# Kernel optimization log

Measured on AMD Instinct MI355X. Metric: run time of the kernel, lower is better.

Reference implementation:

```python
import jax, jax.numpy as jnp
import numpy as np

# Model dims (must match init_kwargs / input_specs)
D = 64          # hidden_dims
L = 2           # num_layer
R = 50          # num_relation
N_RAW = 20000   # num_nodes (module uses num_nodes+1 internally, node 0 = padding)
N = N_RAW + 1
A = 6           # max_arity
E = 30000       # num hyperedges
B = 4           # batch size
C = 500         # candidates per query (1 true + negatives, all differ in one slot)
ARITY = 4       # query arity (constant per batch, as the asserts require)
FEAT = 2 * D    # feature_dim = hidden_dims + input_dim
LN_EPS = 1e-5


def _sinusoidal_pos(max_arity, dim):
    # static_positional_encoding: frozen sinusoidal table, row 0 zeroed (padding)
    pos = np.arange(max_arity + 1, dtype=np.float64)[:, None]
    i = np.arange(dim, dtype=np.float64)[None, :]
    angle = pos / np.power(10000.0, (2.0 * np.floor(i / 2.0)) / dim)
    pe = np.where(np.arange(dim)[None, :] % 2 == 0, np.sin(angle), np.cos(angle))
    pe[0] = 0.0
    return jnp.asarray(pe, jnp.float32)


def setup_inputs() -> dict:
    key = jax.random.key(0)
    ks = jax.random.split(key, 16)
    # --- query batch: one corrupted slot per row, constant relation / arity per row ---
    base = jax.random.randint(ks[0], (B, A), 1, N)                       # entity ids 1..N-1
    base = base * (jnp.arange(A)[None, :] < ARITY)                       # pad slots >= arity -> node 0
    pos_corrupt = jax.random.randint(ks[1], (B,), 0, ARITY)              # which slot differs
    cand = (jnp.arange(C)[None, :] + jax.random.randint(ks[2], (B, 1), 1, N)) % (N - 1) + 1  # [B,C] distinct ids
    ent = jnp.broadcast_to(base[:, None, :], (B, C, A))
    entities_idx = jnp.where(jnp.arange(A)[None, None, :] == pos_corrupt[:, None, None],
                             cand[:, :, None], ent).astype(jnp.int64)    # [B,C,A]
    r_idx = jnp.broadcast_to(jax.random.randint(ks[3], (B, 1), 0, R), (B, C)).astype(jnp.int64)
    arity = jnp.full((B, C), ARITY, dtype=jnp.int64)
    # --- hypergraph: padded incidence lists ---
    edge_ar = jax.random.randint(ks[4], (E,), 2, A + 1)
    edge_list = (jax.random.randint(ks[5], (E, A), 1, N)
                 * (jnp.arange(A)[None, :] < edge_ar[:, None])).astype(jnp.int64)  # [E,A], 0-padded
    rel_list = jax.random.randint(ks[6], (E,), 0, R).astype(jnp.int64)
    # --- parameters ---
    sD = 1.0 / np.sqrt(D)
    sF = 1.0 / np.sqrt(FEAT)
    params = dict(
        query_emb=jax.random.normal(ks[7], (R, D), jnp.float32) * sD,
        rel_emb=jax.random.normal(ks[8], (L, R, D), jnp.float32) * sD,   # per-layer relation table (dependent=False)
        W_agg=jax.random.normal(ks[9], (L, D, D), jnp.float32) * sD,
        W_self=jax.random.normal(ks[10], (L, D, D), jnp.float32) * sD,
        b_lin=jnp.zeros((L, D), jnp.float32),
        ln_g=jnp.ones((L, D), jnp.float32),
        ln_b=jnp.zeros((L, D), jnp.float32),
        W1=jax.random.normal(ks[11], (FEAT, FEAT), jnp.float32) * sF,
        b1=jnp.zeros((FEAT,), jnp.float32),
        W2=jax.random.normal(ks[12], (FEAT, 1), jnp.float32) * sF,
        b2=jnp.zeros((1,), jnp.float32),
    )
    return dict(r_idx=r_idx, entities_idx=entities_idx, arity=arity,
                edge_list=edge_list, rel_list=rel_list,
                pos_table=_sinusoidal_pos(A, D), **params)


def _layer_norm(x, g, b):
    mu = x.mean(-1, keepdims=True)
    var = jnp.mean(jnp.square(x - mu), -1, keepdims=True)
    return (x - mu) * jax.lax.rsqrt(var + LN_EPS) * g + b


def reference(r_idx, entities_idx, arity, edge_list, rel_list, pos_table,
              query_emb, rel_emb, W_agg, W_self, b_lin, ln_g, ln_b, W1, b1, W2, b2):
    all_idx = jnp.transpose(entities_idx, (0, 2, 1))                 # [B,A,C]
    mask_for_diff = jnp.all(all_idx[:, :, :1] == all_idx, axis=-1)   # [B,A] True = slot constant
    pos_search = jnp.argmax(~mask_for_diff, axis=1)                  # [B] corrupted slot
    query = query_emb[r_idx[:, 0]]                                   # [B,D]

    rng = jnp.arange(A)
    valid = rng[None, :] < arity[:, :1]                              # [B,A]
    result = (valid & (rng[None, :] != pos_search[:, None])).astype(all_idx.dtype)  # [B,A]
    idx_ws = all_idx[:, :, 0] * result                               # [B,A] node ids (0 = skip)
    b_ix = jnp.arange(r_idx.shape[0])

    # init: scatter-add relation query + positional encodings onto the query entities
    init = jnp.zeros((r_idx.shape[0], N, D), jnp.float32)
    init = init.at[b_ix[:, None], idx_ws].add(
        jnp.broadcast_to(query[:, None, :], (r_idx.shape[0], A, D)))
    pos_src = pos_table[result * (rng + 1)[None, :]]                 # [B,A,D]
    init = init.at[b_ix[:, None], idx_ws].add(pos_src)
    init = init.at[:, 0, :].set(0.0)                                 # padding node stays 0

    ev = (edge_list != 0)                                            # [E,A] valid slots
    pos_e = pos_table[jnp.arange(1, A + 1)[None, :] * ev]            # [E,A,D] (pos_table[0]=0)
    evf = ev[None, :, :, None].astype(jnp.float32)

    layer_input = init
    for l in range(L):
        h_e = layer_input[:, edge_list]                              # [B,E,A,D] gather
        r_e = rel_emb[l][rel_list]                                   # [E,D]
        m = (h_e + pos_e[None]) * r_e[None, :, None, :] * evf        # per-slot message factor
        msg = (m.sum(axis=2, keepdims=True) - m) * evf               # sum over other slots j != i
        agg = jnp.zeros_like(layer_input).at[:, edge_list].add(msg)  # scatter-add to nodes
        agg = agg.at[:, 0, :].set(0.0)
        out = agg @ W_agg[l] + layer_input @ W_self[l] + b_lin[l]
        out = _layer_norm(out, ln_g[l], ln_b[l])                     # (dropout = identity at eval)
        hidden = jax.nn.relu(out)
        layer_input = hidden + layer_input                           # short_cut residual

    # gather candidate rows (exactly one differing slot per batch row -> jit-friendly)
    cand = jnp.take_along_axis(all_idx, pos_search[:, None, None], axis=1)[:, 0, :]  # [B,C]
    feat_nodes = layer_input[b_ix[:, None], cand]                    # [B,C,D]
    feat = jnp.concatenate(
        [feat_nodes, jnp.broadcast_to(query[:, None, :], feat_nodes.shape)], axis=-1)  # [B,C,2D]
    score = (jax.nn.relu(feat @ W1 + b1) @ W2 + b2)[..., 0]          # [B,C]
    return score
```

## Files before the change

### kernel.cpp

```cpp
#include <hip/hip_runtime.h>

#define D_ 64
#define L_ 2
#define R_ 50
#define N_ 20001
#define A_ 6
#define E_ 30000
#define B_ 4
#define C_ 500
#define FEAT_ 128
#define SC_CAP 8192
#define DCAP 64

__device__ __forceinline__ float rlane(float v, int k) {
  return __builtin_bit_cast(float, __builtin_amdgcn_readlane(__builtin_bit_cast(int, v), k));
}
__device__ __forceinline__ float wave_sum(float v) {
#pragma unroll
  for (int off = 32; off; off >>= 1) v += __shfl_xor(v, off);
  return v;
}
__device__ __forceinline__ float sel6(float p0, float p1, float p2, float p3,
                                      float p4, float p5, int a) {
  float r = p0;
  r = (a == 1) ? p1 : r; r = (a == 2) ? p2 : r; r = (a == 3) ? p3 : r;
  r = (a == 4) ? p4 : r; r = (a == 5) ? p5 : r;
  return r;
}


#define ZQUADS 15007

__global__ void zero_kernel(float4* __restrict__ z) {
  int i = blockIdx.x * blockDim.x + threadIdx.x;
  if (i < ZQUADS) z[i] = make_float4(0.f, 0.f, 0.f, 0.f);
}


#define IB_INIT 4
#define IB_EMASK ((E_ + 255) / 256)
#define IB_BUCKET ((E_ * A_ + 255) / 256)
#define IB_BLOCKS (IB_INIT + IB_EMASK + IB_BUCKET)

__global__ __launch_bounds__(256) void init_bucket_kernel(
    const int* __restrict__ r_idx, const int* __restrict__ ents,
    const int* __restrict__ arity, const float* __restrict__ pos_table,
    const float* __restrict__ query_emb, const int* __restrict__ edge_list,
    int* __restrict__ seednode, float* __restrict__ seedvec,
    int* __restrict__ dirtyA, int* __restrict__ dirty_n, int* __restrict__ meta,
    int* __restrict__ deg, int* __restrict__ bucket, int* __restrict__ emask) {
  __shared__ int diff[A_];
  int bid = blockIdx.x, t = threadIdx.x;
  if (bid < IB_INIT) {
    int b = bid;
    if (t < A_) diff[t] = 0;
    __syncthreads();
#pragma unroll
    for (int a = 0; a < A_; ++a) {
      int v0 = ents[(b * C_) * A_ + a];
      int dd = 0;
      for (int c = t; c < C_; c += 256) dd |= (ents[(b * C_ + c) * A_ + a] != v0);
      if (dd) diff[a] = 1;
    }
    __syncthreads();
    int ps = 0;
    for (int a = A_ - 1; a >= 0; --a) if (diff[a]) ps = a;
    int qr = r_idx[b * C_];
    if (t == 0) { meta[b] = ps; meta[B_ + b] = qr; }
    int ar = arity[b * C_];
    int lane = t & 63;
    for (int a = (t >> 6); a < A_; a += 4) {
      int slot = b * A_ + a;
      if (a < ar && a != ps) {
        int n = ents[(b * C_) * A_ + a];
        seedvec[slot * D_ + lane] = query_emb[qr * D_ + lane] + pos_table[(a + 1) * D_ + lane];
        if (lane == 0) {
          seednode[slot] = n;
          atomicOr(&dirtyA[n], 1 << b);
          atomicOr(&dirty_n[n], 1 << b);
        }
      } else {
        if (lane == 0) seednode[slot] = 0;
      }
    }
  } else if (bid < IB_INIT + IB_EMASK) {
    int e = (bid - IB_INIT) * 256 + t;
    if (e < E_) {
      int msk = 0;
#pragma unroll
      for (int a = 0; a < A_; ++a)
        if (edge_list[e * A_ + a]) msk |= 1 << a;
      emask[e] = msk;
    }
  } else {
    int i = (bid - IB_INIT - IB_EMASK) * 256 + t;
    if (i < E_ * A_) {
      int n = edge_list[i];
      if (n) {
        int slot = atomicAdd(&deg[n], 1);
        if (slot < DCAP) bucket[n * DCAP + slot] = i;
      }
    }
  }
}


#define MAIN_BLOCKS ((N_ + 31) / 32)
#define EPS_BLOCKS ((E_ + 3) / 4)

__global__ __launch_bounds__(256) void main_eps_kernel(
    const int* __restrict__ deg, const int* __restrict__ bucket,
    const int* __restrict__ edge_list, const int* __restrict__ rel_list,
    const int* __restrict__ emask,
    const float* __restrict__ pos_table, const float* __restrict__ rel_emb_l,
    float* __restrict__ H1,
    const float* __restrict__ Wa, const float* __restrict__ bl_,
    const float* __restrict__ g_, const float* __restrict__ be_,
    const int* __restrict__ dirtyA, int* __restrict__ dirty_n,
    const int* __restrict__ seednode, const float* __restrict__ seedvec,
    float* __restrict__ Scorr, unsigned short* __restrict__ emap,
    int* __restrict__ ctrs) {
  __shared__ float A_lds[32 * 68];
  __shared__ float B_lds[64 * 64];
  int t = threadIdx.x;
  int wv = t >> 6, l = t & 63;

  if (blockIdx.x >= MAIN_BLOCKS) {
    int e = (blockIdx.x - MAIN_BLOCKS) * 4 + wv;
    if (e >= E_) return;
    int mem[A_];
    int m = 0;
#pragma unroll
    for (int a = 0; a < A_; ++a) {
      mem[a] = edge_list[e * A_ + a];
      if (mem[a]) m |= dirtyA[mem[a]];
    }
    if (!m) {
      if (l == 0) *reinterpret_cast<unsigned long long*>(&emap[e * B_]) = 0ull;
      return;
    }
    if (l == 0) *reinterpret_cast<unsigned long long*>(&emap[e * B_]) = 0ull;
#pragma unroll
    for (int a = 0; a < A_; ++a)
      if (l == a && mem[a]) atomicOr(&dirty_n[mem[a]], m);
    float rel = rel_emb_l[rel_list[e] * D_ + l];
#pragma unroll
    for (int b = 0; b < B_; ++b) {
      if ((m >> b) & 1) {
        float s = 0.f;
#pragma unroll
        for (int a = 0; a < A_; ++a) {
          if (mem[a]) {
#pragma unroll
            for (int j = 0; j < A_; ++j) {
              int sl = b * A_ + j;
              if (seednode[sl] == mem[a]) s += seedvec[sl * D_ + l];
            }
          }
        }
        int slot = 0;
        if (l == 0) slot = atomicAdd(&ctrs[1], 1);
        slot = __shfl(slot, 0);
        if (slot < SC_CAP) {
          Scorr[slot * D_ + l] = rel * s;
          if (l == 0) emap[e * B_ + b] = (unsigned short)(slot + 1);
        }
      }
    }
    return;
  }

  int m0 = blockIdx.x * 32;
  int ty = t >> 4, tx = t & 15;

  float pv0 = pos_table[1 * D_ + l], pv1 = pos_table[2 * D_ + l];
  float pv2 = pos_table[3 * D_ + l], pv3 = pos_table[4 * D_ + l];
  float pv4 = pos_table[5 * D_ + l], pv5 = pos_table[6 * D_ + l];

#pragma unroll
  for (int it = 0; it < 4; ++it) {
    int idx = t + 256 * it;
    reinterpret_cast<float4*>(B_lds)[idx] = reinterpret_cast<const float4*>(Wa)[idx];
  }

  for (int q = 0; q < 8; ++q) {
    int li = wv * 8 + q;
    int n = m0 + li;
    float aggv = 0.f;
    if (n < N_) {
      int dg = __builtin_amdgcn_readfirstlane(deg[n]);
      int base = n * DCAP;
      for (int p = 0; p < dg; p += 8) {
        int cnt = dg - p;
        int idx8[8];
#pragma unroll
        for (int u = 0; u < 8; ++u) idx8[u] = (u < cnt) ? bucket[base + p + u] : -1;
#pragma unroll
        for (int u = 0; u < 8; ++u) {
          if (idx8[u] >= 0) {
            int e = idx8[u] / 6, a = idx8[u] - e * 6;
            int msk = emask[e];
            float rel = rel_emb_l[rel_list[e] * D_ + l];
            float possum = 0.f;
            possum += (msk & 1) ? pv0 : 0.f;
            possum += (msk & 2) ? pv1 : 0.f;
            possum += (msk & 4) ? pv2 : 0.f;
            possum += (msk & 8) ? pv3 : 0.f;
            possum += (msk & 16) ? pv4 : 0.f;
            possum += (msk & 32) ? pv5 : 0.f;
            float pa = sel6(pv0, pv1, pv2, pv3, pv4, pv5, a);
            aggv = fmaf(rel, possum - pa, aggv);
          }
        }
      }
    }
    A_lds[li * 68 + l] = aggv;
  }
  __syncthreads();

  float acc[2][4];
  float4 bl4 = *reinterpret_cast<const float4*>(&bl_[tx * 4]);
#pragma unroll
  for (int i = 0; i < 2; ++i) {
    acc[i][0] = bl4.x; acc[i][1] = bl4.y; acc[i][2] = bl4.z; acc[i][3] = bl4.w;
  }
#pragma unroll 8
  for (int k = 0; k < 64; ++k) {
    float4 b4 = *reinterpret_cast<const float4*>(&B_lds[k * 64 + tx * 4]);
    float a0 = A_lds[(ty * 2 + 0) * 68 + k];
    float a1 = A_lds[(ty * 2 + 1) * 68 + k];
    acc[0][0] = fmaf(a0, b4.x, acc[0][0]); acc[0][1] = fmaf(a0, b4.y, acc[0][1]);
    acc[0][2] = fmaf(a0, b4.z, acc[0][2]); acc[0][3] = fmaf(a0, b4.w, acc[0][3]);
    acc[1][0] = fmaf(a1, b4.x, acc[1][0]); acc[1][1] = fmaf(a1, b4.y, acc[1][1]);
    acc[1][2] = fmaf(a1, b4.z, acc[1][2]); acc[1][3] = fmaf(a1, b4.w, acc[1][3]);
  }
  __syncthreads();
#pragma unroll
  for (int i = 0; i < 2; ++i) {
    float4 v = make_float4(acc[i][0], acc[i][1], acc[i][2], acc[i][3]);
    *reinterpret_cast<float4*>(&A_lds[(ty * 2 + i) * 68 + tx * 4]) = v;
  }
  __syncthreads();

  float g = g_[l], be = be_[l];
#pragma unroll 4
  for (int rr = 0; rr < 8; ++rr) {
    int r = wv * 8 + rr;
    int n = m0 + r;
    float x = A_lds[r * 68 + l];
    float mu = wave_sum(x) * (1.f / 64.f);
    float dx = x - mu;
    float var = wave_sum(dx * dx) * (1.f / 64.f);
    float y = dx * rsqrtf(var + 1e-5f) * g + be;
    if (n < N_) H1[n * D_ + l] = fmaxf(y, 0.f);
  }
}


__global__ __launch_bounds__(256) void corr_kernel(
    const int* __restrict__ deg, const int* __restrict__ bucket,
    const int* __restrict__ rel_list, const int* __restrict__ emask,
    const float* __restrict__ pos_table, const float* __restrict__ rel_emb_l,
    const float* __restrict__ Scorr, const unsigned short* __restrict__ emap,
    const int* __restrict__ dirty_n,
    const int* __restrict__ seednode, const float* __restrict__ seedvec,
    int* __restrict__ cmap, float* __restrict__ Hcorr,
    const float* __restrict__ Wa, const float* __restrict__ Ws,
    const float* __restrict__ bl_, const float* __restrict__ g_,
    const float* __restrict__ be_, int* __restrict__ ctrs) {
  __shared__ float WaL[64 * 64];
  __shared__ float WsL[64 * 64];
  int t = threadIdx.x;
  int wv = t >> 6, lane = t & 63;
  int n = blockIdx.x * 4 + wv;
  int m = (n < N_) ? dirty_n[n] : 0;
  if (__syncthreads_or(m) == 0) return;
#pragma unroll
  for (int it = 0; it < 4; ++it) {
    int idx = t + 256 * it;
    reinterpret_cast<float4*>(WaL)[idx] = reinterpret_cast<const float4*>(Wa)[idx];
    reinterpret_cast<float4*>(WsL)[idx] = reinterpret_cast<const float4*>(Ws)[idx];
  }
  __syncthreads();
  if (!m) return;

  float pv0 = pos_table[1 * D_ + lane], pv1 = pos_table[2 * D_ + lane];
  float pv2 = pos_table[3 * D_ + lane], pv3 = pos_table[4 * D_ + lane];
  float pv4 = pos_table[5 * D_ + lane], pv5 = pos_table[6 * D_ + lane];

  int slot = 0;
  if (lane == 0) slot = atomicAdd(&ctrs[2], 1);
  slot = __shfl(slot, 0);
  if (lane == 0) cmap[n] = slot;

  float blv = bl_[lane], gv = g_[lane], bev = be_[lane];
  int dg = deg[n];
  int base = n * DCAP;
  float ss0 = 0.f, ss1 = 0.f, ss2 = 0.f, ss3 = 0.f;
  float rs = 0.f, ps = 0.f;
  for (int p = 0; p < dg; ++p) {
    int ii = bucket[base + p];
    int e = ii / 6, a = ii - e * 6;
    int msk = emask[e];
    float rel = rel_emb_l[rel_list[e] * D_ + lane];
    float possum = 0.f;
    possum += (msk & 1) ? pv0 : 0.f;
    possum += (msk & 2) ? pv1 : 0.f;
    possum += (msk & 4) ? pv2 : 0.f;
    possum += (msk & 8) ? pv3 : 0.f;
    possum += (msk & 16) ? pv4 : 0.f;
    possum += (msk & 32) ? pv5 : 0.f;
    float base_v = rel * possum;
    rs += rel;
    ps = fmaf(rel, sel6(pv0, pv1, pv2, pv3, pv4, pv5, a), ps);
    if ((m >> 0) & 1) { int ei = emap[e * B_ + 0]; ss0 += base_v + (ei ? Scorr[(ei - 1) * D_ + lane] : 0.f); }
    if ((m >> 1) & 1) { int ei = emap[e * B_ + 1]; ss1 += base_v + (ei ? Scorr[(ei - 1) * D_ + lane] : 0.f); }
    if ((m >> 2) & 1) { int ei = emap[e * B_ + 2]; ss2 += base_v + (ei ? Scorr[(ei - 1) * D_ + lane] : 0.f); }
    if ((m >> 3) & 1) { int ei = emap[e * B_ + 3]; ss3 += base_v + (ei ? Scorr[(ei - 1) * D_ + lane] : 0.f); }
  }
#pragma unroll
  for (int b = 0; b < B_; ++b) {
    if ((m >> b) & 1) {
      float ssb = (b == 0) ? ss0 : (b == 1) ? ss1 : (b == 2) ? ss2 : ss3;
      float hv = 0.f;
#pragma unroll
      for (int j = 0; j < A_; ++j) {
        int sl = b * A_ + j;
        if (seednode[sl] == n) hv += seedvec[sl * D_ + lane];
      }
      float aggv = ssb - hv * rs - ps;
      float out = blv;
#pragma unroll 16
      for (int k = 0; k < 64; ++k) {
        out = fmaf(rlane(aggv, k), WaL[k * 64 + lane], out);
        out = fmaf(rlane(hv, k), WsL[k * 64 + lane], out);
      }
      float mu = wave_sum(out) * (1.f / 64.f);
      float dx = out - mu;
      float var = wave_sum(dx * dx) * (1.f / 64.f);
      float y = dx * rsqrtf(var + 1e-5f) * gv + bev;
      Hcorr[(slot * B_ + b) * D_ + lane] = fmaxf(y, 0.f) + hv;
    }
  }
}


__global__ __launch_bounds__(512) void cand_kernel(
    const int* __restrict__ ents, const int* __restrict__ meta,
    const int* __restrict__ deg, const int* __restrict__ bucket,
    const int* __restrict__ edge_list, const int* __restrict__ rel_list,
    const float* __restrict__ pos_table, const float* __restrict__ rel_emb_l,
    const float* __restrict__ H1, const float* __restrict__ Hcorr,
    const int* __restrict__ cmap, const int* __restrict__ dirty_n,
    const float* __restrict__ query_emb,
    const float* __restrict__ Wa, const float* __restrict__ Ws,
    const float* __restrict__ bl_, const float* __restrict__ g_,
    const float* __restrict__ be_,
    const float* __restrict__ W1, const float* __restrict__ b1,
    const float* __restrict__ W2, const float* __restrict__ b2,
    float* __restrict__ out) {
  __shared__ float WaL[64 * 64];
  __shared__ float WsL[64 * 64];
  int t = threadIdx.x;
#pragma unroll
  for (int it = 0; it < 2; ++it) {
    int idx = t + 512 * it;
    reinterpret_cast<float4*>(WaL)[idx] = reinterpret_cast<const float4*>(Wa)[idx];
    reinterpret_cast<float4*>(WsL)[idx] = reinterpret_cast<const float4*>(Ws)[idx];
  }
  __syncthreads();
  int w = blockIdx.x * 8 + (t >> 6);
  int lane = t & 63;
  if (w >= B_ * C_) return;
  int b = w / C_;
  int c = w - b * C_;
  int psn = meta[b];
  int qr = meta[B_ + b];
  int n = ents[(b * C_ + c) * A_ + psn];

  float pv0 = pos_table[1 * D_ + lane], pv1 = pos_table[2 * D_ + lane];
  float pv2 = pos_table[3 * D_ + lane], pv3 = pos_table[4 * D_ + lane];
  float pv4 = pos_table[5 * D_ + lane], pv5 = pos_table[6 * D_ + lane];

  float h1v = H1[n * D_ + lane];
  if ((dirty_n[n] >> b) & 1) h1v = Hcorr[(cmap[n] * B_ + b) * D_ + lane];

  int dg = __builtin_amdgcn_readfirstlane(deg[n]);
  int base = n * DCAP;
  float aggv = 0.f;
  for (int p = 0; p < dg; ++p) {
    int ii = bucket[base + p];
    int e = ii / 6, a = ii - e * 6;
    float rel = rel_emb_l[rel_list[e] * D_ + lane];
    float s = 0.f;
#pragma unroll
    for (int a2 = 0; a2 < A_; ++a2) {
      int m2 = edge_list[e * A_ + a2];
      if (m2) {
        float hm = H1[m2 * D_ + lane];
        if ((dirty_n[m2] >> b) & 1) hm = Hcorr[(cmap[m2] * B_ + b) * D_ + lane];
        float pa2 = sel6(pv0, pv1, pv2, pv3, pv4, pv5, a2);
        s += hm + pa2;
      }
    }
    float pa = sel6(pv0, pv1, pv2, pv3, pv4, pv5, a);
    aggv = fmaf(s - h1v - pa, rel, aggv);
  }

  float outv = bl_[lane];
#pragma unroll 16
  for (int k = 0; k < 64; ++k) {
    outv = fmaf(rlane(aggv, k), WaL[k * 64 + lane], outv);
    outv = fmaf(rlane(h1v, k), WsL[k * 64 + lane], outv);
  }
  float mu = wave_sum(outv) * (1.f / 64.f);
  float dx = outv - mu;
  float var = wave_sum(dx * dx) * (1.f / 64.f);
  float y = dx * rsqrtf(var + 1e-5f) * g_[lane] + be_[lane];
  float h2v = fmaxf(y, 0.f) + h1v;

  float qv = query_emb[qr * D_ + lane];
  float hid0 = b1[lane];
  float hid1 = b1[D_ + lane];
#pragma unroll
  for (int k = 0; k < D_; ++k) {
    float f = rlane(h2v, k);
    hid0 = fmaf(f, W1[k * FEAT_ + lane], hid0);
    hid1 = fmaf(f, W1[k * FEAT_ + D_ + lane], hid1);
  }
#pragma unroll
  for (int k = 0; k < D_; ++k) {
    float q = rlane(qv, k);
    hid0 = fmaf(q, W1[(D_ + k) * FEAT_ + lane], hid0);
    hid1 = fmaf(q, W1[(D_ + k) * FEAT_ + D_ + lane], hid1);
  }
  float accs = fmaxf(hid0, 0.f) * W2[lane] + fmaxf(hid1, 0.f) * W2[D_ + lane];
  accs = wave_sum(accs);
  if (lane == 0) out[w] = accs + b2[0];
}


extern "C" void kernel_launch(void* const* d_in, const int* in_sizes, int n_in,
                              void* d_out, int out_size, void* d_ws, size_t ws_size,
                              hipStream_t stream) {
  const int* r_idx = (const int*)d_in[0];
  const int* ents = (const int*)d_in[1];
  const int* arity = (const int*)d_in[2];
  const int* edge_list = (const int*)d_in[3];
  const int* rel_list = (const int*)d_in[4];
  const float* pos_table = (const float*)d_in[5];
  const float* query_emb = (const float*)d_in[6];
  const float* rel_emb = (const float*)d_in[7];
  const float* W_agg = (const float*)d_in[8];
  const float* W_self = (const float*)d_in[9];
  const float* b_lin = (const float*)d_in[10];
  const float* ln_g = (const float*)d_in[11];
  const float* ln_b = (const float*)d_in[12];
  const float* W1 = (const float*)d_in[13];
  const float* b1 = (const float*)d_in[14];
  const float* W2 = (const float*)d_in[15];
  const float* b2 = (const float*)d_in[16];
  float* out = (float*)d_out;

  char* ws = (char*)d_ws;
  float* H1      = (float*)(ws + 0);
  float* Hcorr   = (float*)(ws + 5120512);
  float* Scorr   = (float*)(ws + 25601536);
  int* cmap      = (int*)(ws + 27698688);
  int* seednode  = (int*)(ws + 27778816);
  float* seedvec = (float*)(ws + 27778912);
  int* meta      = (int*)(ws + 27785056);
  int* emask     = (int*)(ws + 27785216);
  unsigned short* emap = (unsigned short*)(ws + 27905216);
  int* bucket    = (int*)(ws + 28145280);
  const size_t Z = 33265536;
  int* deg       = (int*)(ws + Z);
  int* dirtyA    = (int*)(ws + Z + 80016);
  int* dirty_n   = (int*)(ws + Z + 160032);
  int* ctrs      = (int*)(ws + Z + 240048);
  const size_t ZBYTES = 240112;
  if (ws_size < Z + ZBYTES) return;

  const float* rel0 = rel_emb;
  const float* rel1 = rel_emb + R_ * D_;

  zero_kernel<<<(ZQUADS + 255) / 256, 256, 0, stream>>>((float4*)(ws + Z));

  init_bucket_kernel<<<IB_BLOCKS, 256, 0, stream>>>(
      r_idx, ents, arity, pos_table, query_emb, edge_list,
      seednode, seedvec, dirtyA, dirty_n, meta, deg, bucket, emask);

  main_eps_kernel<<<MAIN_BLOCKS + EPS_BLOCKS, 256, 0, stream>>>(
      deg, bucket, edge_list, rel_list, emask, pos_table, rel0, H1,
      W_agg, b_lin, ln_g, ln_b,
      dirtyA, dirty_n, seednode, seedvec, Scorr, emap, ctrs);

  corr_kernel<<<(N_ + 3) / 4, 256, 0, stream>>>(
      deg, bucket, rel_list, emask, pos_table, rel0, Scorr, emap,
      dirty_n, seednode, seedvec, cmap, Hcorr,
      W_agg, W_self, b_lin, ln_g, ln_b, ctrs);

  cand_kernel<<<(B_ * C_ + 7) / 8, 512, 0, stream>>>(
      ents, meta, deg, bucket, edge_list, rel_list, pos_table, rel1,
      H1, Hcorr, cmap, dirty_n, query_emb,
      W_agg + D_ * D_, W_self + D_ * D_, b_lin + D_, ln_g + D_, ln_b + D_,
      W1, b1, W2, b2, out);

  (void)in_sizes; (void)n_in; (void)out_size;
}
```

Measured before the change: 113.2 us.

## Precompute per-edge layer-1 message sums and apply sparse dirty corrections in cand kernel

Adds a per-edge pass, fused into the correction kernel launch, that precomputes rel1*(sum of H1 plus positional encodings) for every hyperedge, along with a per-edge dirty mask. The candidate kernel then sums these precomputed edge vectors and only recomputes deltas for edges touching batch-corrupted nodes, instead of gathering all member embeddings per incident edge. The matvec loops are also split into two accumulators for ILP, and the candidate kernel block size drops to 256. In exchange it computes SB1 for all 30000 edges (about 7.7MB written) even though only edges near candidates are needed, which may cost more than it saves.

```diff
diff --git a/kernel.cpp b/kernel.cpp
--- a/kernel.cpp
+++ b/kernel.cpp
@@ -135,11 +135,8 @@
       mem[a] = edge_list[e * A_ + a];
       if (mem[a]) m |= dirtyA[mem[a]];
     }
-    if (!m) {
-      if (l == 0) *reinterpret_cast<unsigned long long*>(&emap[e * B_]) = 0ull;
-      return;
-    }
     if (l == 0) *reinterpret_cast<unsigned long long*>(&emap[e * B_]) = 0ull;
+    if (!m) return;
 #pragma unroll
     for (int a = 0; a < A_; ++a)
       if (l == a && mem[a]) atomicOr(&dirty_n[mem[a]], m);
@@ -257,21 +254,50 @@
 }
 
 
-__global__ __launch_bounds__(256) void corr_kernel(
+#define CORR_BLOCKS ((N_ + 3) / 4)
+#define SB1_BLOCKS ((E_ + 3) / 4)
+
+__global__ __launch_bounds__(256) void corr_sb1_kernel(
     const int* __restrict__ deg, const int* __restrict__ bucket,
-    const int* __restrict__ rel_list, const int* __restrict__ emask,
-    const float* __restrict__ pos_table, const float* __restrict__ rel_emb_l,
+    const int* __restrict__ edge_list, const int* __restrict__ rel_list,
+    const int* __restrict__ emask,
+    const float* __restrict__ pos_table,
+    const float* __restrict__ rel0, const float* __restrict__ rel1,
     const float* __restrict__ Scorr, const unsigned short* __restrict__ emap,
     const int* __restrict__ dirty_n,
     const int* __restrict__ seednode, const float* __restrict__ seedvec,
+    const float* __restrict__ H1,
     int* __restrict__ cmap, float* __restrict__ Hcorr,
+    float* __restrict__ SB1, int* __restrict__ edirty,
     const float* __restrict__ Wa, const float* __restrict__ Ws,
     const float* __restrict__ bl_, const float* __restrict__ g_,
     const float* __restrict__ be_, int* __restrict__ ctrs) {
+  int t = threadIdx.x;
+  int wv = t >> 6, lane = t & 63;
+
+  if (blockIdx.x >= CORR_BLOCKS) {
+    int e = (blockIdx.x - CORR_BLOCKS) * 4 + wv;
+    if (e >= E_) return;
+    int mem[A_];
+#pragma unroll
+    for (int a = 0; a < A_; ++a) mem[a] = edge_list[e * A_ + a];
+    int ed = 0;
+    float s = 0.f;
+#pragma unroll
+    for (int a = 0; a < A_; ++a) {
+      if (mem[a]) {
+        ed |= dirty_n[mem[a]];
+        s += H1[mem[a] * D_ + lane] + pos_table[(a + 1) * D_ + lane];
+      }
+    }
+    float rel = rel1[rel_list[e] * D_ + lane];
+    SB1[e * D_ + lane] = rel * s;
+    if (lane == 0) edirty[e] = ed;
+    return;
+  }
+
   __shared__ float WaL[64 * 64];
   __shared__ float WsL[64 * 64];
-  int t = threadIdx.x;
-  int wv = t >> 6, lane = t & 63;
   int n = blockIdx.x * 4 + wv;
   int m = (n < N_) ? dirty_n[n] : 0;
   if (__syncthreads_or(m) == 0) return;
@@ -302,7 +328,7 @@
     int ii = bucket[base + p];
     int e = ii / 6, a = ii - e * 6;
     int msk = emask[e];
-    float rel = rel_emb_l[rel_list[e] * D_ + lane];
+    float rel = rel0[rel_list[e] * D_ + lane];
     float possum = 0.f;
     possum += (msk & 1) ? pv0 : 0.f;
     possum += (msk & 2) ? pv1 : 0.f;
@@ -329,12 +355,15 @@
         if (seednode[sl] == n) hv += seedvec[sl * D_ + lane];
       }
       float aggv = ssb - hv * rs - ps;
-      float out = blv;
-#pragma unroll 16
-      for (int k = 0; k < 64; ++k) {
-        out = fmaf(rlane(aggv, k), WaL[k * 64 + lane], out);
-        out = fmaf(rlane(hv, k), WsL[k * 64 + lane], out);
-      }
+      float out0 = blv, out1 = 0.f;
+#pragma unroll
+      for (int k = 0; k < 64; k += 2) {
+        out0 = fmaf(rlane(aggv, k), WaL[k * 64 + lane], out0);
+        out0 = fmaf(rlane(hv, k), WsL[k * 64 + lane], out0);
+        out1 = fmaf(rlane(aggv, k + 1), WaL[(k + 1) * 64 + lane], out1);
+        out1 = fmaf(rlane(hv, k + 1), WsL[(k + 1) * 64 + lane], out1);
+      }
+      float out = out0 + out1;
       float mu = wave_sum(out) * (1.f / 64.f);
       float dx = out - mu;
       float var = wave_sum(dx * dx) * (1.f / 64.f);
@@ -345,13 +374,14 @@
 }
 
 
-__global__ __launch_bounds__(512) void cand_kernel(
+__global__ __launch_bounds__(256) void cand_kernel(
     const int* __restrict__ ents, const int* __restrict__ meta,
     const int* __restrict__ deg, const int* __restrict__ bucket,
     const int* __restrict__ edge_list, const int* __restrict__ rel_list,
     const float* __restrict__ pos_table, const float* __restrict__ rel_emb_l,
     const float* __restrict__ H1, const float* __restrict__ Hcorr,
     const int* __restrict__ cmap, const int* __restrict__ dirty_n,
+    const float* __restrict__ SB1, const int* __restrict__ edirty,
     const float* __restrict__ query_emb,
     const float* __restrict__ Wa, const float* __restrict__ Ws,
     const float* __restrict__ bl_, const float* __restrict__ g_,
@@ -363,13 +393,13 @@
   __shared__ float WsL[64 * 64];
   int t = threadIdx.x;
 #pragma unroll
-  for (int it = 0; it < 2; ++it) {
-    int idx = t + 512 * it;
+  for (int it = 0; it < 4; ++it) {
+    int idx = t + 256 * it;
     reinterpret_cast<float4*>(WaL)[idx] = reinterpret_cast<const float4*>(Wa)[idx];
     reinterpret_cast<float4*>(WsL)[idx] = reinterpret_cast<const float4*>(Ws)[idx];
   }
   __syncthreads();
-  int w = blockIdx.x * 8 + (t >> 6);
+  int w = blockIdx.x * 4 + (t >> 6);
   int lane = t & 63;
   if (w >= B_ * C_) return;
   int b = w / C_;
@@ -387,32 +417,38 @@
 
   int dg = __builtin_amdgcn_readfirstlane(deg[n]);
   int base = n * DCAP;
-  float aggv = 0.f;
+  float ss = 0.f, rs = 0.f, ps = 0.f;
   for (int p = 0; p < dg; ++p) {
     int ii = bucket[base + p];
     int e = ii / 6, a = ii - e * 6;
+    float sb = SB1[e * D_ + lane];
     float rel = rel_emb_l[rel_list[e] * D_ + lane];
-    float s = 0.f;
-#pragma unroll
-    for (int a2 = 0; a2 < A_; ++a2) {
-      int m2 = edge_list[e * A_ + a2];
-      if (m2) {
-        float hm = H1[m2 * D_ + lane];
-        if ((dirty_n[m2] >> b) & 1) hm = Hcorr[(cmap[m2] * B_ + b) * D_ + lane];
-        float pa2 = sel6(pv0, pv1, pv2, pv3, pv4, pv5, a2);
-        s += hm + pa2;
-      }
-    }
-    float pa = sel6(pv0, pv1, pv2, pv3, pv4, pv5, a);
-    aggv = fmaf(s - h1v - pa, rel, aggv);
-  }
-
-  float outv = bl_[lane];
-#pragma unroll 16
-  for (int k = 0; k < 64; ++k) {
-    outv = fmaf(rlane(aggv, k), WaL[k * 64 + lane], outv);
-    outv = fmaf(rlane(h1v, k), WsL[k * 64 + lane], outv);
-  }
+    int ed = edirty[e];
+    if ((ed >> b) & 1) {
+      float sdelta = 0.f;
+#pragma unroll
+      for (int a2 = 0; a2 < A_; ++a2) {
+        int m2 = edge_list[e * A_ + a2];
+        if (m2 && ((dirty_n[m2] >> b) & 1))
+          sdelta += Hcorr[(cmap[m2] * B_ + b) * D_ + lane] - H1[m2 * D_ + lane];
+      }
+      sb = fmaf(rel, sdelta, sb);
+    }
+    ss += sb;
+    rs += rel;
+    ps = fmaf(rel, sel6(pv0, pv1, pv2, pv3, pv4, pv5, a), ps);
+  }
+  float aggv = ss - h1v * rs - ps;
+
+  float out0 = bl_[lane], out1 = 0.f;
+#pragma unroll
+  for (int k = 0; k < 64; k += 2) {
+    out0 = fmaf(rlane(aggv, k), WaL[k * 64 + lane], out0);
+    out0 = fmaf(rlane(h1v, k), WsL[k * 64 + lane], out0);
+    out1 = fmaf(rlane(aggv, k + 1), WaL[(k + 1) * 64 + lane], out1);
+    out1 = fmaf(rlane(h1v, k + 1), WsL[(k + 1) * 64 + lane], out1);
+  }
+  float outv = out0 + out1;
   float mu = wave_sum(outv) * (1.f / 64.f);
   float dx = outv - mu;
   float var = wave_sum(dx * dx) * (1.f / 64.f);
@@ -420,20 +456,25 @@
   float h2v = fmaxf(y, 0.f) + h1v;
 
   float qv = query_emb[qr * D_ + lane];
-  float hid0 = b1[lane];
-  float hid1 = b1[D_ + lane];
-#pragma unroll
-  for (int k = 0; k < D_; ++k) {
-    float f = rlane(h2v, k);
-    hid0 = fmaf(f, W1[k * FEAT_ + lane], hid0);
-    hid1 = fmaf(f, W1[k * FEAT_ + D_ + lane], hid1);
-  }
-#pragma unroll
-  for (int k = 0; k < D_; ++k) {
-    float q = rlane(qv, k);
-    hid0 = fmaf(q, W1[(D_ + k) * FEAT_ + lane], hid0);
-    hid1 = fmaf(q, W1[(D_ + k) * FEAT_ + D_ + lane], hid1);
-  }
+  float h0a = b1[lane], h0b = 0.f;
+  float h1a = b1[D_ + lane], h1b = 0.f;
+#pragma unroll
+  for (int k = 0; k < 64; k += 2) {
+    float f0 = rlane(h2v, k), f1 = rlane(h2v, k + 1);
+    h0a = fmaf(f0, W1[k * FEAT_ + lane], h0a);
+    h1a = fmaf(f0, W1[k * FEAT_ + D_ + lane], h1a);
+    h0b = fmaf(f1, W1[(k + 1) * FEAT_ + lane], h0b);
+    h1b = fmaf(f1, W1[(k + 1) * FEAT_ + D_ + lane], h1b);
+  }
+#pragma unroll
+  for (int k = 0; k < 64; k += 2) {
+    float q0 = rlane(qv, k), q1 = rlane(qv, k + 1);
+    h0a = fmaf(q0, W1[(D_ + k) * FEAT_ + lane], h0a);
+    h1a = fmaf(q0, W1[(D_ + k) * FEAT_ + D_ + lane], h1a);
+    h0b = fmaf(q1, W1[(D_ + k + 1) * FEAT_ + lane], h0b);
+    h1b = fmaf(q1, W1[(D_ + k + 1) * FEAT_ + D_ + lane], h1b);
+  }
+  float hid0 = h0a + h0b, hid1 = h1a + h1b;
   float accs = fmaxf(hid0, 0.f) * W2[lane] + fmaxf(hid1, 0.f) * W2[D_ + lane];
   accs = wave_sum(accs);
   if (lane == 0) out[w] = accs + b2[0];
@@ -479,7 +520,9 @@
   int* dirty_n   = (int*)(ws + Z + 160032);
   int* ctrs      = (int*)(ws + Z + 240048);
   const size_t ZBYTES = 240112;
-  if (ws_size < Z + ZBYTES) return;
+  float* SB1     = (float*)(ws + 33600000);
+  int* edirty    = (int*)(ws + 41280000);
+  if (ws_size < 41400016) return;
 
   const float* rel0 = rel_emb;
   const float* rel1 = rel_emb + R_ * D_;
@@ -495,14 +538,15 @@
       W_agg, b_lin, ln_g, ln_b,
       dirtyA, dirty_n, seednode, seedvec, Scorr, emap, ctrs);
 
-  corr_kernel<<<(N_ + 3) / 4, 256, 0, stream>>>(
-      deg, bucket, rel_list, emask, pos_table, rel0, Scorr, emap,
-      dirty_n, seednode, seedvec, cmap, Hcorr,
+  corr_sb1_kernel<<<CORR_BLOCKS + SB1_BLOCKS, 256, 0, stream>>>(
+      deg, bucket, edge_list, rel_list, emask, pos_table, rel0, rel1,
+      Scorr, emap, dirty_n, seednode, seedvec, H1,
+      cmap, Hcorr, SB1, edirty,
       W_agg, W_self, b_lin, ln_g, ln_b, ctrs);
 
-  cand_kernel<<<(B_ * C_ + 7) / 8, 512, 0, stream>>>(
+  cand_kernel<<<(B_ * C_ + 3) / 4, 256, 0, stream>>>(
       ents, meta, deg, bucket, edge_list, rel_list, pos_table, rel1,
-      H1, Hcorr, cmap, dirty_n, query_emb,
+      H1, Hcorr, cmap, dirty_n, SB1, edirty, query_emb,
       W_agg + D_ * D_, W_self + D_ * D_, b_lin + D_, ln_g + D_, ln_b + D_,
       W1, b1, W2, b2, out);
 
```

New measurement: 113.2 us. No clear change (+0.0%).
